# Performance work log

Measured on AMD Instinct MI355X. Metric: run time of the kernel, lower is better.

The kernel has to match this reference:

```python
import jax, jax.numpy as jnp
import numpy as np

# Dims: b=2, C=256 (in_channels), IC=128 (inter_channels), H=W=64, N=4096
B, C, IC, H, W = 2, 256, 128, 64, 64
N = H * W
K_RATIO = 0.5
BN_EPS = 1e-5


def setup_inputs() -> dict:
    key = jax.random.key(0)
    ks = jax.random.split(key, 12)
    s = 0.05
    return {
        "x": jax.random.normal(ks[0], (B, C, H, W), dtype=jnp.float32),
        "hard_map": jax.random.uniform(ks[1], (B, 1, H, W), dtype=jnp.float32),
        # 1x1 conv weights stored as (out_ch, in_ch)
        "Wg": jax.random.normal(ks[2], (IC, C), dtype=jnp.float32) * s,
        "bg": jnp.zeros((IC,), dtype=jnp.float32),
        "Wth": jax.random.normal(ks[3], (IC, C), dtype=jnp.float32) * s,
        "bth": jnp.zeros((IC,), dtype=jnp.float32),
        "Wph": jax.random.normal(ks[4], (IC, C), dtype=jnp.float32) * s,
        "bph": jnp.zeros((IC,), dtype=jnp.float32),
        # GCN weight: inter -> inter
        "Wgcn": jax.random.normal(ks[5], (IC, IC), dtype=jnp.float32) * s,
        # w_gcn: 1x1 conv inter -> in_channels, then BatchNorm affine
        "Wout": jax.random.normal(ks[6], (C, IC), dtype=jnp.float32) * s,
        "bout": jnp.zeros((C,), dtype=jnp.float32),
        "gamma": jnp.ones((C,), dtype=jnp.float32),
        "beta": jnp.zeros((C,), dtype=jnp.float32),
    }


def _conv1x1(x, Wc, bc):
    # x: (b, cin, H, W), Wc: (cout, cin)
    return jnp.einsum("bchw,oc->bohw", x, Wc) + bc[None, :, None, None]


def reference(x, hard_map, Wg, bg, Wth, bth, Wph, bph, Wgcn, Wout, bout, gamma, beta):
    b, c, h, w = x.shape
    n = h * w
    ic = Wg.shape[0]

    # g/theta/phi 1x1 projections, flattened to nodes
    g_x = _conv1x1(x, Wg, bg).reshape(b, ic, n).transpose(0, 2, 1)      # (b, N, IC)
    theta_x = _conv1x1(x, Wth, bth).reshape(b, ic, n).transpose(0, 2, 1)  # (b, N, IC)
    phi_x = _conv1x1(x, Wph, bph).reshape(b, ic, n)                      # (b, IC, N)

    # Dense non-local attention, softmax over keys
    att = jax.nn.softmax(jnp.einsum("bnc,bcm->bnm", theta_x, phi_x), axis=-1)  # (b,N,N)

    # grid_2_COO (no_grad in torch): keep top-k entries per row (k = k_ratio*N),
    # restrict rows to 'hard' pixels from hard_map, row-renormalize.
    k = int(K_RATIO * n)
    kth = jax.lax.top_k(att, k)[0][..., -1:]                  # (b,N,1) k-th largest per row
    hard = (hard_map.reshape(b, n) > 0.5).astype(att.dtype)   # (b,N) hard-pixel mask
    A = jnp.where(att >= kth, att, jnp.zeros((), att.dtype)) * hard[:, :, None]
    A = A / (A.sum(axis=-1, keepdims=True) + 1e-6)
    A = jax.lax.stop_gradient(A)  # built under torch.no_grad

    # GCN: relu(A (X W))
    gc = jax.nn.relu(jnp.einsum("bnm,bmc->bnc", A, g_x @ Wgcn))  # (b,N,IC)

    # back to image layout, w_gcn 1x1 conv + BatchNorm (training-mode stats)
    gc = gc.reshape(b, h, w, ic).transpose(0, 3, 1, 2)  # (b,IC,H,W)
    y = _conv1x1(gc, Wout, bout)                        # (b,C,H,W)
    mean = y.mean(axis=(0, 2, 3))
    var = y.var(axis=(0, 2, 3))
    y = (y - mean[None, :, None, None]) * jax.lax.rsqrt(var + BN_EPS)[None, :, None, None]
    y = gamma[None, :, None, None] * y + beta[None, :, None, None]

    return x + y
```

## Files before the change

kernel.cpp:

```cpp
#include <hip/hip_runtime.h>

#define B_ 2
#define C_ 256
#define IC_ 128
#define N_ 4096
#define KSEL 2048
#define KS_PV 8

#define OFF_GC    0u
#define OFF_Y     1048576u
#define OFF_MEAN  3145728u
#define OFF_RSIG  3145984u
#define OFF_CNT   3146240u
#define OFF_LIST  3146304u
#define OFF_RANK  3154496u
#define OFF_THB   3162688u
#define OFF_PHB   3686976u
#define OFF_GWT   4211264u
#define OFF_XTH   4735552u
#define OFF_WALL  5784128u
#define OFF_BALL  5833280u
#define OFF_S     5833664u

typedef __attribute__((ext_vector_type(8))) _Float16 f16x8;
typedef __attribute__((ext_vector_type(4))) float f32x4;

__device__ __forceinline__ unsigned short f2h(float f) {
    union { _Float16 h; unsigned short u; } cv;
    cv.h = (_Float16)f;
    return cv.u;
}
__device__ __forceinline__ float h2f(unsigned short u) {
    union { unsigned short u; _Float16 h; } cv;
    cv.u = u;
    return (float)cv.h;
}

__global__ __launch_bounds__(256) void prep_kernel(
    const float* __restrict__ x, unsigned short* __restrict__ xTH,
    const float* __restrict__ Wth, const float* __restrict__ bth,
    const float* __restrict__ Wg,  const float* __restrict__ bg,
    const float* __restrict__ Wgcn,
    const float* __restrict__ Wph, const float* __restrict__ bph,
    unsigned short* __restrict__ WallH, float* __restrict__ ball,
    const float* __restrict__ hard_map, int* __restrict__ cnt,
    int* __restrict__ list, int* __restrict__ rank)
{
    __shared__ float Xs[64][65];
    __shared__ int wsum[4];
    const int bid = blockIdx.x;
    const int t = threadIdx.x;

    if (bid < 512) {
        const int n0 = (bid & 63) * 64;
        const int c0 = ((bid >> 6) & 3) * 64;
        const int b  = bid >> 8;
#pragma unroll
        for (int s = 0; s < 4; ++s) {
            int e4 = t + 256 * s;
            int cc = e4 >> 4, c4 = e4 & 15;
            float4 v = *(const float4*)&x[((size_t)b * C_ + c0 + cc) * N_ + n0 + c4 * 4];
            Xs[cc][c4 * 4 + 0] = v.x; Xs[cc][c4 * 4 + 1] = v.y;
            Xs[cc][c4 * 4 + 2] = v.z; Xs[cc][c4 * 4 + 3] = v.w;
        }
        __syncthreads();
#pragma unroll
        for (int s = 0; s < 4; ++s) {
            int e = t + 256 * s;
            int nn = e >> 4, c4 = e & 15;
            ushort4 h;
            h.x = f2h(Xs[c4 * 4 + 0][nn]);
            h.y = f2h(Xs[c4 * 4 + 1][nn]);
            h.z = f2h(Xs[c4 * 4 + 2][nn]);
            h.w = f2h(Xs[c4 * 4 + 3][nn]);
            *(ushort4*)&xTH[((size_t)b * N_ + n0 + nn) * C_ + c0 + c4 * 4] = h;
        }
    } else if (bid < 896) {
        const int o = bid - 512;
        const int c = t;
        const int oo = o & 127;
        float wv, bv;
        if (o < 128) {
            wv = Wth[oo * C_ + c];
            bv = bth[oo];
        } else if (o < 256) {
            float acc = 0.f;
            for (int i = 0; i < IC_; ++i)
                acc = fmaf(Wgcn[i * IC_ + oo], Wg[i * C_ + c], acc);
            wv = acc;
            float bacc = 0.f;
            for (int i = 0; i < IC_; ++i)
                bacc = fmaf(Wgcn[i * IC_ + oo], bg[i], bacc);
            bv = bacc;
        } else {
            wv = Wph[oo * C_ + c];
            bv = bph[oo];
        }
        WallH[o * C_ + c] = f2h(wv);
        if (c == 0) ball[o] = bv;
    } else {
        const int b = bid - 896;
        const int lane = t & 63, wid = t >> 6;
        const float* hm = hard_map + (size_t)b * N_;
        int flags[16];
        int c = 0;
#pragma unroll
        for (int q = 0; q < 4; ++q) {
            float4 v = *(const float4*)&hm[t * 16 + q * 4];
            flags[q * 4 + 0] = v.x > 0.5f;
            flags[q * 4 + 1] = v.y > 0.5f;
            flags[q * 4 + 2] = v.z > 0.5f;
            flags[q * 4 + 3] = v.w > 0.5f;
            c += flags[q * 4] + flags[q * 4 + 1] + flags[q * 4 + 2] + flags[q * 4 + 3];
        }
        int xv = c;
#pragma unroll
        for (int off = 1; off < 64; off <<= 1) {
            int y = __shfl_up(xv, off);
            if (lane >= off) xv += y;
        }
        if (lane == 63) wsum[wid] = xv;
        __syncthreads();
        int base = 0;
        for (int ww = 0; ww < wid; ++ww) base += wsum[ww];
        int pos = base + xv - c;
        int* lst = list + b * N_;
        int* rnk = rank + b * N_;
#pragma unroll
        for (int e = 0; e < 16; ++e) {
            int n = t * 16 + e;
            if (flags[e]) { lst[pos] = n; rnk[n] = pos; ++pos; }
            else rnk[n] = -1;
        }
        if (t == 0) {
            int tot = 0;
#pragma unroll
            for (int ww = 0; ww < 4; ++ww) tot += wsum[ww];
            cnt[b] = tot;
        }
    }
}

__global__ __launch_bounds__(256) void proj_kernel(
    const unsigned short* __restrict__ xTH,
    const unsigned short* __restrict__ WallH, const float* __restrict__ ball,
    unsigned short* __restrict__ thetaH, unsigned short* __restrict__ gWTH,
    unsigned short* __restrict__ phiH)
{
    __shared__ unsigned short Xt[128][72];
    __shared__ unsigned short Wt[128][72];
    const int n0 = blockIdx.x * 128;
    const int pj = blockIdx.y;
    const int b  = blockIdx.z;
    const int t = threadIdx.x, w = t >> 6, lane = t & 63;
    const int lrow = lane & 15, lk = (lane >> 4) * 8;
    const int wA = (w >> 1) * 64, wB = (w & 1) * 64;

    f32x4 acc[4][4];
#pragma unroll
    for (int u = 0; u < 4; ++u)
#pragma unroll
        for (int v = 0; v < 4; ++v) acc[u][v] = (f32x4)(0.f);

    for (int kc = 0; kc < C_; kc += 64) {
        __syncthreads();
#pragma unroll
        for (int s = 0; s < 4; ++s) {
            int e4 = t + 256 * s;
            int r = e4 >> 3, k8 = e4 & 7;
            *(float4*)&Xt[r][k8 * 8] =
                *(const float4*)&xTH[((size_t)b * N_ + n0 + r) * C_ + kc + k8 * 8];
        }
#pragma unroll
        for (int s = 0; s < 4; ++s) {
            int e4 = t + 256 * s;
            int r = e4 >> 3, k8 = e4 & 7;
            *(float4*)&Wt[r][k8 * 8] =
                *(const float4*)&WallH[(size_t)(pj * 128 + r) * C_ + kc + k8 * 8];
        }
        __syncthreads();

#pragma unroll
        for (int kstep = 0; kstep < 2; ++kstep) {
            const int kk = kstep * 32 + lk;
            f16x8 af[4], bf[4];
            if (pj != 1) {
#pragma unroll
                for (int u = 0; u < 4; ++u)
                    af[u] = *(const f16x8*)&Wt[wA + u * 16 + lrow][kk];
#pragma unroll
                for (int v = 0; v < 4; ++v)
                    bf[v] = *(const f16x8*)&Xt[wB + v * 16 + lrow][kk];
            } else {
#pragma unroll
                for (int u = 0; u < 4; ++u)
                    af[u] = *(const f16x8*)&Xt[wA + u * 16 + lrow][kk];
#pragma unroll
                for (int v = 0; v < 4; ++v)
                    bf[v] = *(const f16x8*)&Wt[wB + v * 16 + lrow][kk];
            }
#pragma unroll
            for (int u = 0; u < 4; ++u)
#pragma unroll
                for (int v = 0; v < 4; ++v)
                    acc[u][v] = __builtin_amdgcn_mfma_f32_16x16x32_f16(
                        af[u], bf[v], acc[u][v], 0, 0, 0);
        }
    }

    const int crow = (lane >> 4) * 4;
    if (pj != 1) {
        unsigned short* dst = (pj == 0) ? thetaH : phiH;
        const int bb2 = (pj == 0) ? 0 : 256;
#pragma unroll
        for (int u = 0; u < 4; ++u) {
            const int ob = wA + u * 16 + crow;
            float b0 = ball[bb2 + ob + 0], b1 = ball[bb2 + ob + 1];
            float b2 = ball[bb2 + ob + 2], b3 = ball[bb2 + ob + 3];
#pragma unroll
            for (int v = 0; v < 4; ++v) {
                const int n = n0 + wB + v * 16 + lrow;
                ushort4 h;
                h.x = f2h(acc[u][v][0] + b0);
                h.y = f2h(acc[u][v][1] + b1);
                h.z = f2h(acc[u][v][2] + b2);
                h.w = f2h(acc[u][v][3] + b3);
                *(ushort4*)&dst[((size_t)b * N_ + n) * IC_ + ob] = h;
            }
        }
    } else {
#pragma unroll
        for (int v = 0; v < 4; ++v) {
            const int o = wB + v * 16 + lrow;
            const float bo = ball[128 + o];
#pragma unroll
            for (int u = 0; u < 4; ++u) {
                const int nb = n0 + wA + u * 16 + crow;
                ushort4 h;
                h.x = f2h(acc[u][v][0] + bo);
                h.y = f2h(acc[u][v][1] + bo);
                h.z = f2h(acc[u][v][2] + bo);
                h.w = f2h(acc[u][v][3] + bo);
                *(ushort4*)&gWTH[((size_t)b * IC_ + o) * N_ + nb] = h;
            }
        }
    }
}

__global__ __launch_bounds__(256) void score_kernel(
    const unsigned short* __restrict__ thetaH,
    const unsigned short* __restrict__ phiH,
    const int* __restrict__ cnt, const int* __restrict__ list,
    unsigned short* __restrict__ SH, int r0base, int qr)
{
    __shared__ unsigned short Th[128][136];
    __shared__ unsigned short Ph[128][136];
    __shared__ int sIdx[128];

    const int b = blockIdx.z;
    const int count = cnt[b];
    const int lr0 = blockIdx.y * 128;
    if (r0base + lr0 >= count) return;
    const int m0 = blockIdx.x * 128;
    const int t = threadIdx.x;
    const int w = t >> 6, lane = t & 63;

    if (t < 128) {
        int gr = r0base + lr0 + t;
        sIdx[t] = (gr < count) ? list[b * N_ + gr] : -1;
    }
    __syncthreads();

#pragma unroll
    for (int s = 0; s < 8; ++s) {
        int e4 = t + 256 * s;
        int r = e4 >> 4, k4 = e4 & 15;
        int gr = sIdx[r];
        float4 v = make_float4(0.f, 0.f, 0.f, 0.f);
        if (gr >= 0)
            v = *(const float4*)&thetaH[((size_t)b * N_ + gr) * IC_ + k4 * 8];
        *(float4*)&Th[r][k4 * 8] = v;
    }
#pragma unroll
    for (int s = 0; s < 8; ++s) {
        int e4 = t + 256 * s;
        int r = e4 >> 4, k4 = e4 & 15;
        *(float4*)&Ph[r][k4 * 8] =
            *(const float4*)&phiH[((size_t)b * N_ + m0 + r) * IC_ + k4 * 8];
    }
    __syncthreads();

    const int wm = (w >> 1) * 64, wr = (w & 1) * 64;
    const int lrow = lane & 15, lk = (lane >> 4) * 8;

    f32x4 acc[4][4];
#pragma unroll
    for (int u = 0; u < 4; ++u)
#pragma unroll
        for (int v = 0; v < 4; ++v) acc[u][v] = (f32x4)(0.f);

#pragma unroll
    for (int ks = 0; ks < 4; ++ks) {
        const int kk = ks * 32 + lk;
        f16x8 af[4], bf[4];
#pragma unroll
        for (int u = 0; u < 4; ++u)
            af[u] = *(const f16x8*)&Ph[wm + u * 16 + lrow][kk];
#pragma unroll
        for (int v = 0; v < 4; ++v)
            bf[v] = *(const f16x8*)&Th[wr + v * 16 + lrow][kk];
#pragma unroll
        for (int u = 0; u < 4; ++u)
#pragma unroll
            for (int v = 0; v < 4; ++v)
                acc[u][v] = __builtin_amdgcn_mfma_f32_16x16x32_f16(
                    af[u], bf[v], acc[u][v], 0, 0, 0);
    }

    const int crow = (lane >> 4) * 4;
#pragma unroll
    for (int u = 0; u < 4; ++u) {
        const int mb = m0 + wm + u * 16 + crow;
#pragma unroll
        for (int v = 0; v < 4; ++v) {
            const int r = lr0 + wr + v * 16 + lrow;
            ushort4 h;
            h.x = f2h(acc[u][v][0]);
            h.y = f2h(acc[u][v][1]);
            h.z = f2h(acc[u][v][2]);
            h.w = f2h(acc[u][v][3]);
            *(ushort4*)&SH[((size_t)b * qr + r) * N_ + mb] = h;
        }
    }
}

__global__ __launch_bounds__(256) void select_kernel(
    unsigned short* __restrict__ SH, const int* __restrict__ cnt,
    int r0base, int qr)
{
    __shared__ unsigned int sHist[4][256];
    __shared__ unsigned int sWsum[4];
    __shared__ float sRed[8];
    __shared__ unsigned int sPrefix, sRemain;

    const int b = blockIdx.y;
    const int lr = blockIdx.x;
    if (r0base + lr >= cnt[b]) return;
    const int t = threadIdx.x, lane = t & 63, wid = t >> 6;

    uint4* row = (uint4*)(SH + ((size_t)b * qr + lr) * N_);
    uint4 rv[2];
    rv[0] = row[t];
    rv[1] = row[t + 256];

    float sv[16];
    unsigned int mu[16];
#pragma unroll
    for (int q = 0; q < 2; ++q) {
        const unsigned int* pu = (const unsigned int*)&rv[q];
#pragma unroll
        for (int dw = 0; dw < 4; ++dw) {
            unsigned int u = pu[dw];
            unsigned short h0 = (unsigned short)(u & 0xffffu);
            unsigned short h1 = (unsigned short)(u >> 16);
            int e = q * 8 + dw * 2;
            sv[e]     = h2f(h0);
            sv[e + 1] = h2f(h1);
            mu[e]     = (h0 & 0x8000u) ? (unsigned int)((~h0) & 0xffffu)
                                       : (unsigned int)(h0 | 0x8000u);
            mu[e + 1] = (h1 & 0x8000u) ? (unsigned int)((~h1) & 0xffffu)
                                       : (unsigned int)(h1 | 0x8000u);
        }
    }

    float m = -3.4e38f;
#pragma unroll
    for (int e = 0; e < 16; ++e) m = fmaxf(m, sv[e]);
#pragma unroll
    for (int off = 32; off > 0; off >>= 1) m = fmaxf(m, __shfl_xor(m, off));
    if (lane == 0) sRed[wid] = m;
    __syncthreads();
    m = fmaxf(fmaxf(sRed[0], sRed[1]), fmaxf(sRed[2], sRed[3]));

    unsigned int prefix = 0u;
    unsigned int remain = KSEL;
    for (int d = 1; d >= 0; --d) {
        __syncthreads();
#pragma unroll
        for (int ww = 0; ww < 4; ++ww) sHist[ww][t] = 0u;
        __syncthreads();
#pragma unroll
        for (int e = 0; e < 16; ++e) {
            if ((mu[e] >> (8 * (d + 1))) == prefix)
                atomicAdd(&sHist[wid][(mu[e] >> (8 * d)) & 255u], 1u);
        }
        __syncthreads();
        unsigned int x = sHist[0][t] + sHist[1][t] + sHist[2][t] + sHist[3][t];
        unsigned int own = x;
#pragma unroll
        for (int off = 1; off < 64; off <<= 1) {
            unsigned int y = __shfl_down(x, off);
            if (lane + off < 64) x += y;
        }
        if (lane == 0) sWsum[wid] = x;
        __syncthreads();
        for (int ww = wid + 1; ww < 4; ++ww) x += sWsum[ww];
        unsigned int nxt = x - own;
        if (x >= remain && nxt < remain) {
            sPrefix = (prefix << 8) | (unsigned int)t;
            sRemain = remain - nxt;
        }
        __syncthreads();
        prefix = sPrefix;
        remain = sRemain;
    }
    const unsigned int tu = prefix;

    float z = 0.f, ssel = 0.f;
#pragma unroll
    for (int e = 0; e < 16; ++e) {
        float ex = expf(sv[e] - m);
        z += ex;
        if (mu[e] >= tu) ssel += ex;
    }
#pragma unroll
    for (int off = 32; off > 0; off >>= 1) {
        z    += __shfl_xor(z, off);
        ssel += __shfl_xor(ssel, off);
    }
    __syncthreads();
    if (lane == 0) { sRed[wid] = z; sRed[4 + wid] = ssel; }
    __syncthreads();
    const float zt = sRed[0] + sRed[1] + sRed[2] + sRed[3];
    const float st = sRed[4] + sRed[5] + sRed[6] + sRed[7];
    const float inv = 1.f / (st + 1e-6f * zt);

#pragma unroll
    for (int q = 0; q < 2; ++q) {
        unsigned int* pu = (unsigned int*)&rv[q];
#pragma unroll
        for (int dw = 0; dw < 4; ++dw) {
            int e = q * 8 + dw * 2;
            unsigned int p0 = (mu[e] >= tu) ? (unsigned int)f2h(expf(sv[e] - m) * inv) : 0u;
            unsigned int p1 = (mu[e + 1] >= tu) ? (unsigned int)f2h(expf(sv[e + 1] - m) * inv) : 0u;
            pu[dw] = p0 | (p1 << 16);
        }
    }
    row[t]       = rv[0];
    row[t + 256] = rv[1];
}

__global__ __launch_bounds__(256) void pv_kernel(
    const unsigned short* __restrict__ SH, const unsigned short* __restrict__ gWTH,
    const int* __restrict__ cnt, unsigned short* __restrict__ gc_partH,
    int r0base, int qr)
{
    __shared__ unsigned short Pt[64][72];
    __shared__ unsigned short Gt[128][72];

    const int b = blockIdx.z;
    const int count = cnt[b];
    const int lr0 = blockIdx.x * 64;
    if (r0base + lr0 >= count) return;
    const int ks = blockIdx.y;
    const int t = threadIdx.x;
    const int w = t >> 6, lane = t & 63;
    const int lrow = lane & 15, lk = (lane >> 4) * 8;
    const int wiA = (w & 1) * 64, wrB = (w >> 1) * 32;

    f32x4 acc[4][2];
#pragma unroll
    for (int u = 0; u < 4; ++u)
#pragma unroll
        for (int v = 0; v < 2; ++v) acc[u][v] = (f32x4)(0.f);

    for (int jc = ks * 512; jc < ks * 512 + 512; jc += 64) {
        __syncthreads();
#pragma unroll
        for (int s = 0; s < 2; ++s) {
            int e4 = t + 256 * s;
            int r = e4 >> 3, k8 = e4 & 7;
            *(float4*)&Pt[r][k8 * 8] =
                *(const float4*)&SH[((size_t)b * qr + lr0 + r) * N_ + jc + k8 * 8];
        }
#pragma unroll
        for (int s = 0; s < 4; ++s) {
            int e4 = t + 256 * s;
            int i = e4 >> 3, k8 = e4 & 7;
            *(float4*)&Gt[i][k8 * 8] =
                *(const float4*)&gWTH[((size_t)b * IC_ + i) * N_ + jc + k8 * 8];
        }
        __syncthreads();

#pragma unroll
        for (int kstep = 0; kstep < 2; ++kstep) {
            const int kk = kstep * 32 + lk;
            f16x8 af[4], bf[2];
#pragma unroll
            for (int u = 0; u < 4; ++u)
                af[u] = *(const f16x8*)&Gt[wiA + u * 16 + lrow][kk];
#pragma unroll
            for (int v = 0; v < 2; ++v)
                bf[v] = *(const f16x8*)&Pt[wrB + v * 16 + lrow][kk];
#pragma unroll
            for (int u = 0; u < 4; ++u)
#pragma unroll
                for (int v = 0; v < 2; ++v)
                    acc[u][v] = __builtin_amdgcn_mfma_f32_16x16x32_f16(
                        af[u], bf[v], acc[u][v], 0, 0, 0);
        }
    }

    const int crow = (lane >> 4) * 4;
#pragma unroll
    for (int u = 0; u < 4; ++u) {
        const int ib = wiA + u * 16 + crow;
#pragma unroll
        for (int v = 0; v < 2; ++v) {
            const int r = lr0 + wrB + v * 16 + lrow;
            ushort4 h;
            h.x = f2h(acc[u][v][0]);
            h.y = f2h(acc[u][v][1]);
            h.z = f2h(acc[u][v][2]);
            h.w = f2h(acc[u][v][3]);
            *(ushort4*)&gc_partH[(((size_t)b * KS_PV + ks) * qr + r) * IC_ + ib] = h;
        }
    }
}

__global__ __launch_bounds__(256) void scatter_kernel(
    const unsigned short* __restrict__ gc_partH, const int* __restrict__ rank,
    float* __restrict__ gc, int r0base, int qr)
{
    const int b = blockIdx.y;
    int idx = blockIdx.x * 256 + threadIdx.x;
    int n = idx >> 7, i = idx & 127;
    int r = rank[b * N_ + n];
    if (r < 0) {
        if (r0base == 0) gc[((size_t)b * N_ + n) * IC_ + i] = 0.f;
        return;
    }
    if (r < r0base || r >= r0base + qr) return;
    const int lr = r - r0base;
    float v = 0.f;
#pragma unroll
    for (int ks = 0; ks < KS_PV; ++ks)
        v += h2f(gc_partH[(((size_t)b * KS_PV + ks) * qr + lr) * IC_ + i]);
    gc[((size_t)b * N_ + n) * IC_ + i] = fmaxf(v, 0.f);
}

__global__ __launch_bounds__(256) void y_kernel(
    const float* __restrict__ gc, const float* __restrict__ Wout,
    const float* __restrict__ bout, float* __restrict__ y)
{
    __shared__ float Wt[64][33];
    __shared__ float Gt[32][68];
    const int n0 = blockIdx.x * 64;
    const int c0 = blockIdx.y * 64;
    const int b  = blockIdx.z;
    const int t = threadIdx.x;
    const int tx = t & 15, ty = t >> 4;

    float acc[4][4];
#pragma unroll
    for (int u = 0; u < 4; ++u)
#pragma unroll
        for (int v = 0; v < 4; ++v) acc[u][v] = 0.f;

    for (int kc = 0; kc < IC_; kc += 32) {
        __syncthreads();
#pragma unroll
        for (int s = 0; s < 2; ++s) {
            int e4 = t + 256 * s;
            int c = e4 >> 3, k4 = e4 & 7;
            float4 ww = *(const float4*)&Wout[(size_t)(c0 + c) * IC_ + kc + k4 * 4];
            Wt[c][k4 * 4 + 0] = ww.x; Wt[c][k4 * 4 + 1] = ww.y;
            Wt[c][k4 * 4 + 2] = ww.z; Wt[c][k4 * 4 + 3] = ww.w;
        }
#pragma unroll
        for (int s = 0; s < 2; ++s) {
            int e4 = t + 256 * s;
            int nn = e4 >> 3, k4 = e4 & 7;
            float4 g = *(const float4*)&gc[((size_t)b * N_ + n0 + nn) * IC_ + kc + k4 * 4];
            Gt[k4 * 4 + 0][nn] = g.x; Gt[k4 * 4 + 1][nn] = g.y;
            Gt[k4 * 4 + 2][nn] = g.z; Gt[k4 * 4 + 3][nn] = g.w;
        }
        __syncthreads();

#pragma unroll 4
        for (int k = 0; k < 32; ++k) {
            float a[4];
#pragma unroll
            for (int u = 0; u < 4; ++u) a[u] = Wt[ty * 4 + u][k];
            const float4 g4 = *(const float4*)&Gt[k][tx * 4];
            const float gm[4] = {g4.x, g4.y, g4.z, g4.w};
#pragma unroll
            for (int u = 0; u < 4; ++u)
#pragma unroll
                for (int v = 0; v < 4; ++v)
                    acc[u][v] = fmaf(a[u], gm[v], acc[u][v]);
        }
    }

#pragma unroll
    for (int u = 0; u < 4; ++u) {
        const int c = c0 + ty * 4 + u;
        const float bo = bout[c];
        *(float4*)&y[((size_t)b * C_ + c) * N_ + n0 + tx * 4] =
            make_float4(acc[u][0] + bo, acc[u][1] + bo,
                        acc[u][2] + bo, acc[u][3] + bo);
    }
}

__global__ __launch_bounds__(256) void bn_stats_kernel(
    const float* __restrict__ y, float* __restrict__ mean,
    float* __restrict__ rsig)
{
    __shared__ float sr[8];
    const int c = blockIdx.x, t = threadIdx.x;
    const int lane = t & 63, wid = t >> 6;
    float s = 0.f, ss = 0.f;
    for (int b = 0; b < B_; ++b) {
        const float* yr = y + ((size_t)b * C_ + c) * N_;
        for (int n = t; n < N_; n += 256) {
            float v = yr[n];
            s += v; ss = fmaf(v, v, ss);
        }
    }
#pragma unroll
    for (int off = 32; off > 0; off >>= 1) {
        s  += __shfl_xor(s, off);
        ss += __shfl_xor(ss, off);
    }
    if (lane == 0) { sr[wid] = s; sr[4 + wid] = ss; }
    __syncthreads();
    if (t == 0) {
        float st  = sr[0] + sr[1] + sr[2] + sr[3];
        float sst = sr[4] + sr[5] + sr[6] + sr[7];
        float mu  = st / (float)(B_ * N_);
        float var = sst / (float)(B_ * N_) - mu * mu;
        mean[c] = mu;
        rsig[c] = rsqrtf(var + 1e-5f);
    }
}

__global__ __launch_bounds__(256) void final_kernel(
    const float* __restrict__ x, const float* __restrict__ y,
    const float* __restrict__ mean, const float* __restrict__ rsig,
    const float* __restrict__ gamma, const float* __restrict__ beta,
    float* __restrict__ out)
{
    int idx = blockIdx.x * 256 + threadIdx.x;
    if (idx >= B_ * C_ * N_) return;
    int c = (idx >> 12) & (C_ - 1);
    out[idx] = x[idx] + fmaf(gamma[c], (y[idx] - mean[c]) * rsig[c], beta[c]);
}

extern "C" void kernel_launch(void* const* d_in, const int* in_sizes, int n_in,
                              void* d_out, int out_size, void* d_ws, size_t ws_size,
                              hipStream_t stream)
{
    const float* x     = (const float*)d_in[0];
    const float* hard  = (const float*)d_in[1];
    const float* Wg    = (const float*)d_in[2];
    const float* bg    = (const float*)d_in[3];
    const float* Wth   = (const float*)d_in[4];
    const float* bth   = (const float*)d_in[5];
    const float* Wph   = (const float*)d_in[6];
    const float* bph   = (const float*)d_in[7];
    const float* Wgcn  = (const float*)d_in[8];
    const float* Wout  = (const float*)d_in[9];
    const float* bout  = (const float*)d_in[10];
    const float* gamma = (const float*)d_in[11];
    const float* beta  = (const float*)d_in[12];
    float* out = (float*)d_out;
    float* ws  = (float*)d_ws;

    float* gc    = ws + OFF_GC;
    float* y     = ws + OFF_Y;
    float* mean  = ws + OFF_MEAN;
    float* rsig  = ws + OFF_RSIG;
    int*   cnt   = (int*)(ws + OFF_CNT);
    int*   list  = (int*)(ws + OFF_LIST);
    int*   rank  = (int*)(ws + OFF_RANK);
    unsigned short* thetaH = (unsigned short*)(ws + OFF_THB);
    unsigned short* phiH   = (unsigned short*)(ws + OFF_PHB);
    unsigned short* gWTH   = (unsigned short*)(ws + OFF_GWT);
    unsigned short* xTH    = (unsigned short*)(ws + OFF_XTH);
    unsigned short* WallH  = (unsigned short*)(ws + OFF_WALL);
    float* ball  = ws + OFF_BALL;
    unsigned short* SH = (unsigned short*)(ws + OFF_S);

    const size_t wsf = ws_size / sizeof(float);
    int qr;
    unsigned short* gc_partH;
    if (wsf >= OFF_S + (size_t)4096 * 6144) {
        qr = 4096; gc_partH = (unsigned short*)(ws + OFF_S + (size_t)4096 * 4096);
    } else if (wsf >= OFF_S + (size_t)2048 * 6144) {
        qr = 2048; gc_partH = (unsigned short*)(ws + OFF_S + (size_t)2048 * 4096);
    } else {
        qr = 1024; gc_partH = (unsigned short*)out;
    }

    prep_kernel<<<dim3(898), 256, 0, stream>>>(
        x, xTH, Wth, bth, Wg, bg, Wgcn, Wph, bph, WallH, ball,
        hard, cnt, list, rank);
    proj_kernel<<<dim3(N_ / 128, 3, B_), 256, 0, stream>>>(
        xTH, WallH, ball, thetaH, gWTH, phiH);

    for (int r0 = 0; r0 < N_; r0 += qr) {
        score_kernel<<<dim3(N_ / 128, qr / 128, B_), 256, 0, stream>>>(
            thetaH, phiH, cnt, list, SH, r0, qr);
        select_kernel<<<dim3(qr, B_), 256, 0, stream>>>(SH, cnt, r0, qr);
        pv_kernel<<<dim3(qr / 64, KS_PV, B_), 256, 0, stream>>>(
            SH, gWTH, cnt, gc_partH, r0, qr);
        scatter_kernel<<<dim3(N_ * IC_ / 256, B_), 256, 0, stream>>>(
            gc_partH, rank, gc, r0, qr);
    }

    y_kernel<<<dim3(N_ / 64, C_ / 64, B_), 256, 0, stream>>>(gc, Wout, bout, y);
    bn_stats_kernel<<<dim3(C_), 256, 0, stream>>>(y, mean, rsig);
    final_kernel<<<dim3(B_ * C_ * N_ / 256), 256, 0, stream>>>(
        x, y, mean, rsig, gamma, beta, out);
}
```

Measured before the change: 129.1 us.

## Fuse score, top-k select, and PV into one on-chip attention kernel

Replaces the four-kernel score/select/pv/scatter pipeline with a single attn_kernel. Each 512-thread block handles 16 hard rows, keeps their full 4096-wide score rows in shared memory, does the radix top-k and softmax per row, then multiplies by gWT and writes gc directly. Zeroing of gc moves into extra prep_kernel blocks, and the rank array goes away. This removes the global round trips of the score matrix and the partial-sum scatter, at the cost of low occupancy from roughly 130KB of shared memory per block and serialized per-row selection with many barriers.

Measured after the change: 297.6 us. +130.4%, slower.

```diff
diff --git a/kernel.cpp b/kernel.cpp
--- a/kernel.cpp
+++ b/kernel.cpp
@@ -5,7 +5,7 @@
 #define IC_ 128
 #define N_ 4096
 #define KSEL 2048
-#define KS_PV 8
+#define SP 4104
 
 #define OFF_GC    0u
 #define OFF_Y     1048576u
@@ -13,14 +13,12 @@
 #define OFF_RSIG  3145984u
 #define OFF_CNT   3146240u
 #define OFF_LIST  3146304u
-#define OFF_RANK  3154496u
-#define OFF_THB   3162688u
-#define OFF_PHB   3686976u
-#define OFF_GWT   4211264u
-#define OFF_XTH   4735552u
-#define OFF_WALL  5784128u
-#define OFF_BALL  5833280u
-#define OFF_S     5833664u
+#define OFF_THB   3154496u
+#define OFF_PHB   3678784u
+#define OFF_GWT   4203072u
+#define OFF_XTH   4727360u
+#define OFF_WALL  5775936u
+#define OFF_BALL  5825088u
 
 typedef __attribute__((ext_vector_type(8))) _Float16 f16x8;
 typedef __attribute__((ext_vector_type(4))) float f32x4;
@@ -44,7 +42,7 @@
     const float* __restrict__ Wph, const float* __restrict__ bph,
     unsigned short* __restrict__ WallH, float* __restrict__ ball,
     const float* __restrict__ hard_map, int* __restrict__ cnt,
-    int* __restrict__ list, int* __restrict__ rank)
+    int* __restrict__ list, float* __restrict__ gc)
 {
     __shared__ float Xs[64][65];
     __shared__ int wsum[4];
@@ -98,7 +96,7 @@
         }
         WallH[o * C_ + c] = f2h(wv);
         if (c == 0) ball[o] = bv;
-    } else {
+    } else if (bid < 898) {
         const int b = bid - 896;
         const int lane = t & 63, wid = t >> 6;
         const float* hm = hard_map + (size_t)b * N_;
@@ -125,12 +123,10 @@
         for (int ww = 0; ww < wid; ++ww) base += wsum[ww];
         int pos = base + xv - c;
         int* lst = list + b * N_;
-        int* rnk = rank + b * N_;
 #pragma unroll
         for (int e = 0; e < 16; ++e) {
             int n = t * 16 + e;
-            if (flags[e]) { lst[pos] = n; rnk[n] = pos; ++pos; }
-            else rnk[n] = -1;
+            if (flags[e]) lst[pos++] = n;
         }
         if (t == 0) {
             int tot = 0;
@@ -138,6 +134,11 @@
             for (int ww = 0; ww < 4; ++ww) tot += wsum[ww];
             cnt[b] = tot;
         }
+    } else {
+        float* g = gc + (size_t)(bid - 898) * 2048;
+        float4 z4 = make_float4(0.f, 0.f, 0.f, 0.f);
+        *(float4*)&g[t * 4] = z4;
+        *(float4*)&g[1024 + t * 4] = z4;
     }
 }
 
@@ -247,306 +248,204 @@
     }
 }
 
-__global__ __launch_bounds__(256) void score_kernel(
+__global__ __launch_bounds__(512, 1) void attn_kernel(
     const unsigned short* __restrict__ thetaH,
     const unsigned short* __restrict__ phiH,
+    const unsigned short* __restrict__ gWTH,
     const int* __restrict__ cnt, const int* __restrict__ list,
-    unsigned short* __restrict__ SH, int r0base, int qr)
+    float* __restrict__ gc)
 {
-    __shared__ unsigned short Th[128][136];
-    __shared__ unsigned short Ph[128][136];
-    __shared__ int sIdx[128];
-
-    const int b = blockIdx.z;
+    __shared__ unsigned short S[16][SP];
+    __shared__ unsigned short Th[16][136];
+    __shared__ unsigned int sHist[8][256];
+    __shared__ unsigned int sWsum[4];
+    __shared__ float sRedM[8], sRedZ[8], sRedS[8];
+    __shared__ unsigned int sPrefix, sRemain;
+    __shared__ int sIdx[16];
+
+    const int b = blockIdx.y;
     const int count = cnt[b];
-    const int lr0 = blockIdx.y * 128;
-    if (r0base + lr0 >= count) return;
-    const int m0 = blockIdx.x * 128;
+    const int r0 = blockIdx.x * 16;
+    if (r0 >= count) return;
     const int t = threadIdx.x;
     const int w = t >> 6, lane = t & 63;
-
-    if (t < 128) {
-        int gr = r0base + lr0 + t;
+    const int lrow = lane & 15, lk4 = lane >> 4, lk = lk4 * 8;
+
+    if (t < 16) {
+        int gr = r0 + t;
         sIdx[t] = (gr < count) ? list[b * N_ + gr] : -1;
     }
     __syncthreads();
-
-#pragma unroll
-    for (int s = 0; s < 8; ++s) {
-        int e4 = t + 256 * s;
-        int r = e4 >> 4, k4 = e4 & 15;
+    if (t < 256) {
+        int r = t >> 4, k8 = t & 15;
         int gr = sIdx[r];
         float4 v = make_float4(0.f, 0.f, 0.f, 0.f);
         if (gr >= 0)
-            v = *(const float4*)&thetaH[((size_t)b * N_ + gr) * IC_ + k4 * 8];
-        *(float4*)&Th[r][k4 * 8] = v;
-    }
-#pragma unroll
-    for (int s = 0; s < 8; ++s) {
-        int e4 = t + 256 * s;
-        int r = e4 >> 4, k4 = e4 & 15;
-        *(float4*)&Ph[r][k4 * 8] =
-            *(const float4*)&phiH[((size_t)b * N_ + m0 + r) * IC_ + k4 * 8];
+            v = *(const float4*)&thetaH[((size_t)b * N_ + gr) * IC_ + k8 * 8];
+        *(float4*)&Th[r][k8 * 8] = v;
     }
     __syncthreads();
 
-    const int wm = (w >> 1) * 64, wr = (w & 1) * 64;
-    const int lrow = lane & 15, lk = (lane >> 4) * 8;
-
-    f32x4 acc[4][4];
-#pragma unroll
-    for (int u = 0; u < 4; ++u)
-#pragma unroll
-        for (int v = 0; v < 4; ++v) acc[u][v] = (f32x4)(0.f);
-
-#pragma unroll
-    for (int ks = 0; ks < 4; ++ks) {
-        const int kk = ks * 32 + lk;
-        f16x8 af[4], bf[4];
-#pragma unroll
-        for (int u = 0; u < 4; ++u)
-            af[u] = *(const f16x8*)&Ph[wm + u * 16 + lrow][kk];
-#pragma unroll
-        for (int v = 0; v < 4; ++v)
-            bf[v] = *(const f16x8*)&Th[wr + v * 16 + lrow][kk];
-#pragma unroll
-        for (int u = 0; u < 4; ++u)
-#pragma unroll
-            for (int v = 0; v < 4; ++v)
-                acc[u][v] = __builtin_amdgcn_mfma_f32_16x16x32_f16(
-                    af[u], bf[v], acc[u][v], 0, 0, 0);
-    }
-
-    const int crow = (lane >> 4) * 4;
-#pragma unroll
-    for (int u = 0; u < 4; ++u) {
-        const int mb = m0 + wm + u * 16 + crow;
-#pragma unroll
-        for (int v = 0; v < 4; ++v) {
-            const int r = lr0 + wr + v * 16 + lrow;
-            ushort4 h;
-            h.x = f2h(acc[u][v][0]);
-            h.y = f2h(acc[u][v][1]);
-            h.z = f2h(acc[u][v][2]);
-            h.w = f2h(acc[u][v][3]);
-            *(ushort4*)&SH[((size_t)b * qr + r) * N_ + mb] = h;
-        }
-    }
-}
-
-__global__ __launch_bounds__(256) void select_kernel(
-    unsigned short* __restrict__ SH, const int* __restrict__ cnt,
-    int r0base, int qr)
-{
-    __shared__ unsigned int sHist[4][256];
-    __shared__ unsigned int sWsum[4];
-    __shared__ float sRed[8];
-    __shared__ unsigned int sPrefix, sRemain;
-
-    const int b = blockIdx.y;
-    const int lr = blockIdx.x;
-    if (r0base + lr >= cnt[b]) return;
-    const int t = threadIdx.x, lane = t & 63, wid = t >> 6;
-
-    uint4* row = (uint4*)(SH + ((size_t)b * qr + lr) * N_);
-    uint4 rv[2];
-    rv[0] = row[t];
-    rv[1] = row[t + 256];
-
-    float sv[16];
-    unsigned int mu[16];
-#pragma unroll
-    for (int q = 0; q < 2; ++q) {
-        const unsigned int* pu = (const unsigned int*)&rv[q];
+    f16x8 bt[4];
+#pragma unroll
+    for (int ks = 0; ks < 4; ++ks)
+        bt[ks] = *(const f16x8*)&Th[lrow][ks * 32 + lk];
+
+    const unsigned short* phiB = phiH + (size_t)b * N_ * IC_;
+    const int mW = w * 512;
+    for (int mt = 0; mt < 32; mt += 2) {
+        const int mb0 = mW + mt * 16, mb1 = mb0 + 16;
+        f16x8 a0[4], a1[4];
+#pragma unroll
+        for (int ks = 0; ks < 4; ++ks) {
+            a0[ks] = *(const f16x8*)&phiB[(size_t)(mb0 + lrow) * IC_ + ks * 32 + lk];
+            a1[ks] = *(const f16x8*)&phiB[(size_t)(mb1 + lrow) * IC_ + ks * 32 + lk];
+        }
+        f32x4 c0 = (f32x4)(0.f), c1 = (f32x4)(0.f);
+#pragma unroll
+        for (int ks = 0; ks < 4; ++ks) {
+            c0 = __builtin_amdgcn_mfma_f32_16x16x32_f16(a0[ks], bt[ks], c0, 0, 0, 0);
+            c1 = __builtin_amdgcn_mfma_f32_16x16x32_f16(a1[ks], bt[ks], c1, 0, 0, 0);
+        }
+        ushort4 h0, h1;
+        h0.x = f2h(c0[0]); h0.y = f2h(c0[1]); h0.z = f2h(c0[2]); h0.w = f2h(c0[3]);
+        h1.x = f2h(c1[0]); h1.y = f2h(c1[1]); h1.z = f2h(c1[2]); h1.w = f2h(c1[3]);
+        *(ushort4*)&S[lrow][mb0 + lk4 * 4] = h0;
+        *(ushort4*)&S[lrow][mb1 + lk4 * 4] = h1;
+    }
+    __syncthreads();
+
+    for (int rr = 0; rr < 16; ++rr) {
+        uint4 rv = *(const uint4*)&S[rr][t * 8];
+        float sv[8];
+        unsigned int mu[8];
+        const unsigned int* pu = (const unsigned int*)&rv;
 #pragma unroll
         for (int dw = 0; dw < 4; ++dw) {
             unsigned int u = pu[dw];
-            unsigned short h0 = (unsigned short)(u & 0xffffu);
-            unsigned short h1 = (unsigned short)(u >> 16);
-            int e = q * 8 + dw * 2;
-            sv[e]     = h2f(h0);
-            sv[e + 1] = h2f(h1);
-            mu[e]     = (h0 & 0x8000u) ? (unsigned int)((~h0) & 0xffffu)
-                                       : (unsigned int)(h0 | 0x8000u);
-            mu[e + 1] = (h1 & 0x8000u) ? (unsigned int)((~h1) & 0xffffu)
-                                       : (unsigned int)(h1 | 0x8000u);
-        }
-    }
-
-    float m = -3.4e38f;
-#pragma unroll
-    for (int e = 0; e < 16; ++e) m = fmaxf(m, sv[e]);
-#pragma unroll
-    for (int off = 32; off > 0; off >>= 1) m = fmaxf(m, __shfl_xor(m, off));
-    if (lane == 0) sRed[wid] = m;
-    __syncthreads();
-    m = fmaxf(fmaxf(sRed[0], sRed[1]), fmaxf(sRed[2], sRed[3]));
-
-    unsigned int prefix = 0u;
-    unsigned int remain = KSEL;
-    for (int d = 1; d >= 0; --d) {
-        __syncthreads();
-#pragma unroll
-        for (int ww = 0; ww < 4; ++ww) sHist[ww][t] = 0u;
-        __syncthreads();
-#pragma unroll
-        for (int e = 0; e < 16; ++e) {
-            if ((mu[e] >> (8 * (d + 1))) == prefix)
-                atomicAdd(&sHist[wid][(mu[e] >> (8 * d)) & 255u], 1u);
-        }
-        __syncthreads();
-        unsigned int x = sHist[0][t] + sHist[1][t] + sHist[2][t] + sHist[3][t];
-        unsigned int own = x;
-#pragma unroll
-        for (int off = 1; off < 64; off <<= 1) {
-            unsigned int y = __shfl_down(x, off);
-            if (lane + off < 64) x += y;
-        }
-        if (lane == 0) sWsum[wid] = x;
-        __syncthreads();
-        for (int ww = wid + 1; ww < 4; ++ww) x += sWsum[ww];
-        unsigned int nxt = x - own;
-        if (x >= remain && nxt < remain) {
-            sPrefix = (prefix << 8) | (unsigned int)t;
-            sRemain = remain - nxt;
-        }
-        __syncthreads();
-        prefix = sPrefix;
-        remain = sRemain;
-    }
-    const unsigned int tu = prefix;
-
-    float z = 0.f, ssel = 0.f;
-#pragma unroll
-    for (int e = 0; e < 16; ++e) {
-        float ex = expf(sv[e] - m);
-        z += ex;
-        if (mu[e] >= tu) ssel += ex;
-    }
-#pragma unroll
-    for (int off = 32; off > 0; off >>= 1) {
-        z    += __shfl_xor(z, off);
-        ssel += __shfl_xor(ssel, off);
-    }
-    __syncthreads();
-    if (lane == 0) { sRed[wid] = z; sRed[4 + wid] = ssel; }
-    __syncthreads();
-    const float zt = sRed[0] + sRed[1] + sRed[2] + sRed[3];
-    const float st = sRed[4] + sRed[5] + sRed[6] + sRed[7];
-    const float inv = 1.f / (st + 1e-6f * zt);
-
-#pragma unroll
-    for (int q = 0; q < 2; ++q) {
-        unsigned int* pu = (unsigned int*)&rv[q];
+            unsigned short hh0 = (unsigned short)(u & 0xffffu);
+            unsigned short hh1 = (unsigned short)(u >> 16);
+            sv[dw * 2]     = h2f(hh0);
+            sv[dw * 2 + 1] = h2f(hh1);
+            mu[dw * 2]     = (hh0 & 0x8000u) ? (unsigned)((~hh0) & 0xffffu)
+                                             : (unsigned)(hh0 | 0x8000u);
+            mu[dw * 2 + 1] = (hh1 & 0x8000u) ? (unsigned)((~hh1) & 0xffffu)
+                                             : (unsigned)(hh1 | 0x8000u);
+        }
+
+        float m = -3.4e38f;
+#pragma unroll
+        for (int e = 0; e < 8; ++e) m = fmaxf(m, sv[e]);
+#pragma unroll
+        for (int off = 32; off > 0; off >>= 1) m = fmaxf(m, __shfl_xor(m, off));
+        if (lane == 0) sRedM[w] = m;
+        __syncthreads();
+        m = sRedM[0];
+#pragma unroll
+        for (int ww = 1; ww < 8; ++ww) m = fmaxf(m, sRedM[ww]);
+
+        unsigned int prefix = 0u, remain = KSEL;
+        for (int d = 1; d >= 0; --d) {
+            __syncthreads();
+#pragma unroll
+            for (int q = 0; q < 4; ++q)
+                ((unsigned int*)sHist)[t + 512 * q] = 0u;
+            __syncthreads();
+#pragma unroll
+            for (int e = 0; e < 8; ++e)
+                if ((mu[e] >> (8 * (d + 1))) == prefix)
+                    atomicAdd(&sHist[w][(mu[e] >> (8 * d)) & 255u], 1u);
+            __syncthreads();
+            unsigned int x = 0, own = 0;
+            if (t < 256) {
+#pragma unroll
+                for (int ww = 0; ww < 8; ++ww) x += sHist[ww][t];
+                own = x;
+#pragma unroll
+                for (int off = 1; off < 64; off <<= 1) {
+                    unsigned int yv = __shfl_down(x, off);
+                    if (lane + off < 64) x += yv;
+                }
+                if (lane == 0) sWsum[w] = x;
+            }
+            __syncthreads();
+            if (t < 256) {
+                for (int ww = w + 1; ww < 4; ++ww) x += sWsum[ww];
+                unsigned int nxt = x - own;
+                if (x >= remain && nxt < remain) {
+                    sPrefix = (prefix << 8) | (unsigned)t;
+                    sRemain = remain - nxt;
+                }
+            }
+            __syncthreads();
+            prefix = sPrefix;
+            remain = sRemain;
+        }
+        const unsigned int tu = prefix;
+
+        float z = 0.f, ssel = 0.f;
+#pragma unroll
+        for (int e = 0; e < 8; ++e) {
+            float ex = expf(sv[e] - m);
+            z += ex;
+            if (mu[e] >= tu) ssel += ex;
+        }
+#pragma unroll
+        for (int off = 32; off > 0; off >>= 1) {
+            z    += __shfl_xor(z, off);
+            ssel += __shfl_xor(ssel, off);
+        }
+        if (lane == 0) { sRedZ[w] = z; sRedS[w] = ssel; }
+        __syncthreads();
+        float zt = 0.f, st = 0.f;
+#pragma unroll
+        for (int ww = 0; ww < 8; ++ww) { zt += sRedZ[ww]; st += sRedS[ww]; }
+        const float inv = 1.f / (st + 1e-6f * zt);
+
+        uint4 pvv;
+        unsigned int* po = (unsigned int*)&pvv;
 #pragma unroll
         for (int dw = 0; dw < 4; ++dw) {
-            int e = q * 8 + dw * 2;
-            unsigned int p0 = (mu[e] >= tu) ? (unsigned int)f2h(expf(sv[e] - m) * inv) : 0u;
-            unsigned int p1 = (mu[e + 1] >= tu) ? (unsigned int)f2h(expf(sv[e + 1] - m) * inv) : 0u;
-            pu[dw] = p0 | (p1 << 16);
-        }
-    }
-    row[t]       = rv[0];
-    row[t + 256] = rv[1];
-}
-
-__global__ __launch_bounds__(256) void pv_kernel(
-    const unsigned short* __restrict__ SH, const unsigned short* __restrict__ gWTH,
-    const int* __restrict__ cnt, unsigned short* __restrict__ gc_partH,
-    int r0base, int qr)
-{
-    __shared__ unsigned short Pt[64][72];
-    __shared__ unsigned short Gt[128][72];
-
-    const int b = blockIdx.z;
-    const int count = cnt[b];
-    const int lr0 = blockIdx.x * 64;
-    if (r0base + lr0 >= count) return;
-    const int ks = blockIdx.y;
-    const int t = threadIdx.x;
-    const int w = t >> 6, lane = t & 63;
-    const int lrow = lane & 15, lk = (lane >> 4) * 8;
-    const int wiA = (w & 1) * 64, wrB = (w >> 1) * 32;
-
-    f32x4 acc[4][2];
-#pragma unroll
-    for (int u = 0; u < 4; ++u)
-#pragma unroll
-        for (int v = 0; v < 2; ++v) acc[u][v] = (f32x4)(0.f);
-
-    for (int jc = ks * 512; jc < ks * 512 + 512; jc += 64) {
-        __syncthreads();
-#pragma unroll
-        for (int s = 0; s < 2; ++s) {
-            int e4 = t + 256 * s;
-            int r = e4 >> 3, k8 = e4 & 7;
-            *(float4*)&Pt[r][k8 * 8] =
-                *(const float4*)&SH[((size_t)b * qr + lr0 + r) * N_ + jc + k8 * 8];
-        }
-#pragma unroll
-        for (int s = 0; s < 4; ++s) {
-            int e4 = t + 256 * s;
-            int i = e4 >> 3, k8 = e4 & 7;
-            *(float4*)&Gt[i][k8 * 8] =
-                *(const float4*)&gWTH[((size_t)b * IC_ + i) * N_ + jc + k8 * 8];
-        }
-        __syncthreads();
-
-#pragma unroll
-        for (int kstep = 0; kstep < 2; ++kstep) {
-            const int kk = kstep * 32 + lk;
-            f16x8 af[4], bf[2];
-#pragma unroll
-            for (int u = 0; u < 4; ++u)
-                af[u] = *(const f16x8*)&Gt[wiA + u * 16 + lrow][kk];
-#pragma unroll
-            for (int v = 0; v < 2; ++v)
-                bf[v] = *(const f16x8*)&Pt[wrB + v * 16 + lrow][kk];
-#pragma unroll
-            for (int u = 0; u < 4; ++u)
-#pragma unroll
-                for (int v = 0; v < 2; ++v)
-                    acc[u][v] = __builtin_amdgcn_mfma_f32_16x16x32_f16(
-                        af[u], bf[v], acc[u][v], 0, 0, 0);
-        }
-    }
-
-    const int crow = (lane >> 4) * 4;
-#pragma unroll
-    for (int u = 0; u < 4; ++u) {
-        const int ib = wiA + u * 16 + crow;
-#pragma unroll
-        for (int v = 0; v < 2; ++v) {
-            const int r = lr0 + wrB + v * 16 + lrow;
-            ushort4 h;
-            h.x = f2h(acc[u][v][0]);
-            h.y = f2h(acc[u][v][1]);
-            h.z = f2h(acc[u][v][2]);
-            h.w = f2h(acc[u][v][3]);
-            *(ushort4*)&gc_partH[(((size_t)b * KS_PV + ks) * qr + r) * IC_ + ib] = h;
-        }
-    }
-}
-
-__global__ __launch_bounds__(256) void scatter_kernel(
-    const unsigned short* __restrict__ gc_partH, const int* __restrict__ rank,
-    float* __restrict__ gc, int r0base, int qr)
-{
-    const int b = blockIdx.y;
-    int idx = blockIdx.x * 256 + threadIdx.x;
-    int n = idx >> 7, i = idx & 127;
-    int r = rank[b * N_ + n];
-    if (r < 0) {
-        if (r0base == 0) gc[((size_t)b * N_ + n) * IC_ + i] = 0.f;
-        return;
-    }
-    if (r < r0base || r >= r0base + qr) return;
-    const int lr = r - r0base;
-    float v = 0.f;
-#pragma unroll
-    for (int ks = 0; ks < KS_PV; ++ks)
-        v += h2f(gc_partH[(((size_t)b * KS_PV + ks) * qr + lr) * IC_ + i]);
-    gc[((size_t)b * N_ + n) * IC_ + i] = fmaxf(v, 0.f);
+            unsigned int p0 = (mu[dw * 2] >= tu)
+                ? (unsigned)f2h(expf(sv[dw * 2] - m) * inv) : 0u;
+            unsigned int p1 = (mu[dw * 2 + 1] >= tu)
+                ? (unsigned)f2h(expf(sv[dw * 2 + 1] - m) * inv) : 0u;
+            po[dw] = p0 | (p1 << 16);
+        }
+        *(uint4*)&S[rr][t * 8] = pvv;
+        __syncthreads();
+    }
+
+    const unsigned short* gWB = gWTH + ((size_t)b * IC_ + w * 16 + lrow) * N_;
+    f32x4 pa0 = (f32x4)(0.f), pa1 = (f32x4)(0.f);
+    f32x4 pa2 = (f32x4)(0.f), pa3 = (f32x4)(0.f);
+    for (int j = 0; j < N_; j += 128) {
+        f16x8 g0 = *(const f16x8*)&gWB[j + lk];
+        f16x8 g1 = *(const f16x8*)&gWB[j + 32 + lk];
+        f16x8 g2 = *(const f16x8*)&gWB[j + 64 + lk];
+        f16x8 g3 = *(const f16x8*)&gWB[j + 96 + lk];
+        f16x8 p0 = *(const f16x8*)&S[lrow][j + lk];
+        f16x8 p1 = *(const f16x8*)&S[lrow][j + 32 + lk];
+        f16x8 p2 = *(const f16x8*)&S[lrow][j + 64 + lk];
+        f16x8 p3 = *(const f16x8*)&S[lrow][j + 96 + lk];
+        pa0 = __builtin_amdgcn_mfma_f32_16x16x32_f16(g0, p0, pa0, 0, 0, 0);
+        pa1 = __builtin_amdgcn_mfma_f32_16x16x32_f16(g1, p1, pa1, 0, 0, 0);
+        pa2 = __builtin_amdgcn_mfma_f32_16x16x32_f16(g2, p2, pa2, 0, 0, 0);
+        pa3 = __builtin_amdgcn_mfma_f32_16x16x32_f16(g3, p3, pa3, 0, 0, 0);
+    }
+    f32x4 tot = pa0 + pa1;
+    tot = tot + pa2;
+    tot = tot + pa3;
+
+    const int n = sIdx[lrow];
+    if (n >= 0) {
+        float4 o;
+        o.x = fmaxf(tot[0], 0.f);
+        o.y = fmaxf(tot[1], 0.f);
+        o.z = fmaxf(tot[2], 0.f);
+        o.w = fmaxf(tot[3], 0.f);
+        *(float4*)&gc[((size_t)b * N_ + n) * IC_ + w * 16 + lk4 * 4] = o;
+    }
 }
 
 __global__ __launch_bounds__(256) void y_kernel(
@@ -682,42 +581,20 @@
     float* rsig  = ws + OFF_RSIG;
     int*   cnt   = (int*)(ws + OFF_CNT);
     int*   list  = (int*)(ws + OFF_LIST);
-    int*   rank  = (int*)(ws + OFF_RANK);
     unsigned short* thetaH = (unsigned short*)(ws + OFF_THB);
     unsigned short* phiH   = (unsigned short*)(ws + OFF_PHB);
     unsigned short* gWTH   = (unsigned short*)(ws + OFF_GWT);
     unsigned short* xTH    = (unsigned short*)(ws + OFF_XTH);
     unsigned short* WallH  = (unsigned short*)(ws + OFF_WALL);
     float* ball  = ws + OFF_BALL;
-    unsigned short* SH = (unsigned short*)(ws + OFF_S);
-
-    const size_t wsf = ws_size / sizeof(float);
-    int qr;
-    unsigned short* gc_partH;
-    if (wsf >= OFF_S + (size_t)4096 * 6144) {
-        qr = 4096; gc_partH = (unsigned short*)(ws + OFF_S + (size_t)4096 * 4096);
-    } else if (wsf >= OFF_S + (size_t)2048 * 6144) {
-        qr = 2048; gc_partH = (unsigned short*)(ws + OFF_S + (size_t)2048 * 4096);
-    } else {
-        qr = 1024; gc_partH = (unsigned short*)out;
-    }
-
-    prep_kernel<<<dim3(898), 256, 0, stream>>>(
+
+    prep_kernel<<<dim3(1410), 256, 0, stream>>>(
         x, xTH, Wth, bth, Wg, bg, Wgcn, Wph, bph, WallH, ball,
-        hard, cnt, list, rank);
+        hard, cnt, list, gc);
     proj_kernel<<<dim3(N_ / 128, 3, B_), 256, 0, stream>>>(
         xTH, WallH, ball, thetaH, gWTH, phiH);
-
-    for (int r0 = 0; r0 < N_; r0 += qr) {
-        score_kernel<<<dim3(N_ / 128, qr / 128, B_), 256, 0, stream>>>(
-            thetaH, phiH, cnt, list, SH, r0, qr);
-        select_kernel<<<dim3(qr, B_), 256, 0, stream>>>(SH, cnt, r0, qr);
-        pv_kernel<<<dim3(qr / 64, KS_PV, B_), 256, 0, stream>>>(
-            SH, gWTH, cnt, gc_partH, r0, qr);
-        scatter_kernel<<<dim3(N_ * IC_ / 256, B_), 256, 0, stream>>>(
-            gc_partH, rank, gc, r0, qr);
-    }
-
+    attn_kernel<<<dim3(N_ / 16, B_), 512, 0, stream>>>(
+        thetaH, phiH, gWTH, cnt, list, gc);
     y_kernel<<<dim3(N_ / 64, C_ / 64, B_), 256, 0, stream>>>(gc, Wout, bout, y);
     bn_stats_kernel<<<dim3(C_), 256, 0, stream>>>(y, mean, rsig);
     final_kernel<<<dim3(B_ * C_ * N_ / 256), 256, 0, stream>>>(
```
